# Kernel tuning notes

Measured on AMD Instinct MI355X. Metric: run time of the kernel, lower is better.

## Reference

```python
import jax, jax.numpy as jnp
import numpy as np
import math

DEPTH = 4
IN_FEATURES = 1024
LEAF_WIDTH = 256
OUT_FEATURES = 1024
BATCH = 8192
N_LEAVES = 2 ** DEPTH      # 16
N_NODES = 2 ** DEPTH - 1   # 15


def setup_inputs() -> dict:
    key = jax.random.key(0)
    ks = jax.random.split(key, 8)
    l1 = 1.0 / math.sqrt(IN_FEATURES)
    l2 = 1.0 / math.sqrt(LEAF_WIDTH)
    u = lambda k, shape, f: jax.random.uniform(k, shape, jnp.float32, -f, f)
    return {
        "x": jax.random.normal(ks[0], (BATCH, IN_FEATURES), jnp.float32),
        "node_weights": u(ks[1], (N_NODES, IN_FEATURES), l1),
        "node_biases": u(ks[2], (N_NODES, 1), l1),
        "w1s": u(ks[3], (N_LEAVES, IN_FEATURES, LEAF_WIDTH), l1),
        "b1s": u(ks[4], (N_LEAVES, LEAF_WIDTH), l1),
        "w2s": u(ks[5], (N_LEAVES, LEAF_WIDTH, OUT_FEATURES), l2),
        "b2s": u(ks[6], (N_LEAVES, OUT_FEATURES), l2),
    }


def reference(x, node_weights, node_biases, w1s, b1s, w2s, b2s):
    # Soft tree-gated routing (training_forward, soft decisions, no leak).
    B = x.shape[0]
    mixture = jnp.ones((B, N_LEAVES), dtype=x.dtype)
    for d in range(DEPTH):  # static small loop over tree depth
        plat, nxt = 2 ** d - 1, 2 ** (d + 1) - 1
        n = 2 ** d
        w = node_weights[plat:nxt]          # (n, F)
        b = node_biases[plat:nxt]           # (n, 1)
        logits = x @ w.T + b.T              # (B, n)
        be = jax.nn.sigmoid(logits)
        # interleave (1-be, be) along node axis -> (B, 2n, 1)
        mod = jnp.stack([1.0 - be, be], axis=-1).reshape(B, 2 * n, 1)
        mixture = (mixture.reshape(B, 2 * n, N_LEAVES // (2 * n)) * mod).reshape(B, N_LEAVES)
    # Per-leaf two-layer MLP, then mixture-weighted sum over leaves.
    h = jnp.einsum("bf,lfh->blh", x, w1s) + b1s[None]          # (B, L, H)
    a = jax.nn.relu(h)
    y = jnp.einsum("blh,lho->blo", a, w2s) + b2s[None]          # (B, L, O)
    return jnp.sum(y * mixture[:, :, None], axis=1)             # (B, O)
```

## Files before the change

kernel.cpp:

```cpp
#include <hip/hip_runtime.h>
#include <hip/hip_bf16.h>
#include <math.h>

#define BATCH 8192
#define INF   1024
#define LEAFW 256
#define OUTF  1024
#define NLEAF 16
#define NNODE 15
#define NTOT  4096
#define KEXT  4160

typedef __bf16 bf16;
typedef __bf16 bf16x4 __attribute__((ext_vector_type(4)));
typedef __bf16 bf16x8 __attribute__((ext_vector_type(8)));
typedef float  f32x4  __attribute__((ext_vector_type(4)));

#define BM 128
#define BN 128
#define BK 64

__global__ __launch_bounds__(256) void prep_weights_kernel(
    const float* __restrict__ w1, const float* __restrict__ w2,
    const float* __restrict__ b2s, bf16* __restrict__ W1T,
    bf16* __restrict__ W2T) {
  __shared__ float lds[64][65];
  int b = blockIdx.x;
  int t = threadIdx.x;

  if (b < 2048) {
    bool isW1 = b < 1024;
    int bb = isW1 ? b : b - 1024;
    int l = bb >> 6, rem = bb & 63;
    int rb, cb, src_ld;
    const float* src;
    if (isW1) {
      rb = (rem >> 2) * 64; cb = (rem & 3) * 64;
      src = w1 + (size_t)l * INF * LEAFW; src_ld = LEAFW;
    } else {
      rb = (rem >> 4) * 64; cb = (rem & 15) * 64;
      src = w2 + (size_t)l * LEAFW * OUTF; src_ld = OUTF;
    }
    int s4 = t & 15, r = t >> 4;
#pragma unroll
    for (int i = 0; i < 4; ++i) {
      int rr = r + 16 * i;
      float4 v = *reinterpret_cast<const float4*>(
          src + (size_t)(rb + rr) * src_ld + cb + 4 * s4);
      lds[rr][4 * s4 + 0] = v.x;
      lds[rr][4 * s4 + 1] = v.y;
      lds[rr][4 * s4 + 2] = v.z;
      lds[rr][4 * s4 + 3] = v.w;
    }
    __syncthreads();
    int s8 = t & 7, c = t >> 3;
#pragma unroll
    for (int i = 0; i < 2; ++i) {
      int cc = c + 32 * i;
      bf16x8 o;
#pragma unroll
      for (int k = 0; k < 8; ++k) o[k] = (bf16)lds[8 * s8 + k][cc];
      if (isW1)
        *reinterpret_cast<bf16x8*>(
            W1T + (size_t)(l * LEAFW + cb + cc) * INF + rb + 8 * s8) = o;
      else
        *reinterpret_cast<bf16x8*>(
            W2T + (size_t)(cb + cc) * KEXT + l * LEAFW + rb + 8 * s8) = o;
    }
  } else {
    int i = (b - 2048) * 256 + t;
    int o = i >> 6, j = i & 63;
    W2T[(size_t)o * KEXT + NTOT + j] =
        (j < NLEAF) ? (bf16)b2s[(size_t)j * OUTF + o] : (bf16)0.f;
  }
}

__global__ __launch_bounds__(256) void gating_kernel(
    const float4* __restrict__ x4, const float4* __restrict__ nw4,
    const float* __restrict__ nb, float* __restrict__ mg,
    bf16* __restrict__ Aact, bf16x4* __restrict__ Xbf4) {
  int row  = blockIdx.x * 4 + (threadIdx.x >> 6);
  int lane = threadIdx.x & 63;

  float p[NNODE];
#pragma unroll
  for (int j = 0; j < NNODE; ++j) p[j] = 0.f;
#pragma unroll
  for (int c = 0; c < INF / 256; ++c) {
    int idx = c * 64 + lane;
    float4 xv = x4[(size_t)row * (INF / 4) + idx];
#pragma unroll
    for (int j = 0; j < NNODE; ++j) {
      float4 wv = nw4[j * (INF / 4) + idx];
      p[j] += xv.x * wv.x + xv.y * wv.y + xv.z * wv.z + xv.w * wv.w;
    }
    bf16x4 o = {(bf16)xv.x, (bf16)xv.y, (bf16)xv.z, (bf16)xv.w};
    Xbf4[(size_t)row * (INF / 4) + idx] = o;
  }
#pragma unroll
  for (int j = 0; j < NNODE; ++j) {
    float v = p[j];
#pragma unroll
    for (int off = 32; off > 0; off >>= 1) v += __shfl_xor(v, off);
    p[j] = 1.f / (1.f + expf(-(v + nb[j])));
  }
  float mixv[NLEAF];
#pragma unroll
  for (int L = 0; L < NLEAF; ++L) {
    int n1 = 1 + (L >> 3), n2 = 3 + (L >> 2), n3 = 7 + (L >> 1);
    float m = ((L >> 3) & 1) ? p[0] : (1.f - p[0]);
    m *= ((L >> 2) & 1) ? p[n1] : (1.f - p[n1]);
    m *= ((L >> 1) & 1) ? p[n2] : (1.f - p[n2]);
    m *= (L & 1) ? p[n3] : (1.f - p[n3]);
    mixv[L] = m;
  }
  bf16* arow = Aact + (size_t)row * KEXT + NTOT;
  if (lane == 0) {
#pragma unroll
    for (int L = 0; L < NLEAF; ++L) {
      mg[row * NLEAF + L] = mixv[L];
      arow[L] = (bf16)mixv[L];
    }
  }
  if (lane >= 16) arow[lane] = (bf16)0.f;
}

template <int EPI>
__global__ __launch_bounds__(256, 2) void gemm_kernel(
    const bf16* __restrict__ A, int lda, const bf16* __restrict__ BT, int ldb,
    int K, const float* __restrict__ bias, const float* __restrict__ mg,
    bf16* __restrict__ outB, int ldob, float* __restrict__ outF, int ldof) {
  __shared__ __align__(16) bf16 As[BM * BK];
  __shared__ __align__(16) bf16 Bs[BN * BK];

  int t    = threadIdx.x;
  int lane = t & 63;
  int w    = t >> 6;
  int bm   = blockIdx.x * BM;
  int bn   = blockIdx.y * BN;
  int wm   = (w >> 1) * 64;
  int wn   = (w & 1) * 64;

  int sr = t >> 3;
  int sc = t & 7;
  int gc = ((sc ^ (sr & 7)) << 3);

  f32x4 acc[4][4];
#pragma unroll
  for (int i = 0; i < 4; ++i)
#pragma unroll
    for (int j = 0; j < 4; ++j) acc[i][j] = (f32x4){0.f, 0.f, 0.f, 0.f};

  for (int k0 = 0; k0 < K; k0 += BK) {
#pragma unroll
    for (int i = 0; i < 4; ++i) {
      int r = i * 32 + sr;
      __builtin_amdgcn_global_load_lds(
          (const __attribute__((address_space(1))) void*)(
              A + (size_t)(bm + r) * lda + k0 + gc),
          (__attribute__((address_space(3))) void*)((char*)As + i * 4096 +
                                                    t * 16),
          16, 0, 0);
    }
#pragma unroll
    for (int i = 0; i < 4; ++i) {
      int r = i * 32 + sr;
      __builtin_amdgcn_global_load_lds(
          (const __attribute__((address_space(1))) void*)(
              BT + (size_t)(bn + r) * ldb + k0 + gc),
          (__attribute__((address_space(3))) void*)((char*)Bs + i * 4096 +
                                                    t * 16),
          16, 0, 0);
    }
    __syncthreads();

#pragma unroll
    for (int kk = 0; kk < 2; ++kk) {
      int c = (kk * 4 + (lane >> 4)) ^ (lane & 7);
      bf16x8 af[4], bfr[4];
#pragma unroll
      for (int i = 0; i < 4; ++i) {
        int R = wm + i * 16 + (lane & 15);
        af[i] = *reinterpret_cast<const bf16x8*>(&As[R * 64 + c * 8]);
      }
#pragma unroll
      for (int j = 0; j < 4; ++j) {
        int R = wn + j * 16 + (lane & 15);
        bfr[j] = *reinterpret_cast<const bf16x8*>(&Bs[R * 64 + c * 8]);
      }
#pragma unroll
      for (int i = 0; i < 4; ++i)
#pragma unroll
        for (int j = 0; j < 4; ++j)
          acc[i][j] = __builtin_amdgcn_mfma_f32_16x16x32_bf16(
              af[i], bfr[j], acc[i][j], 0, 0, 0);
    }
    __syncthreads();
  }

  int r0 = bm + wm + ((lane >> 4) << 2);
  int c0 = bn + wn + (lane & 15);
  if (EPI == 0) {
    int leaf = (bn + wn) >> 8;
#pragma unroll
    for (int i = 0; i < 4; ++i) {
#pragma unroll
      for (int r = 0; r < 4; ++r) {
        int row = r0 + i * 16 + r;
        float g = mg[row * NLEAF + leaf];
#pragma unroll
        for (int j = 0; j < 4; ++j) {
          int col = c0 + j * 16;
          float v = acc[i][j][r] + bias[col];
          v = v > 0.f ? v : 0.f;
          outB[(size_t)row * ldob + col] = (bf16)(v * g);
        }
      }
    }
  } else {
#pragma unroll
    for (int i = 0; i < 4; ++i)
#pragma unroll
      for (int r = 0; r < 4; ++r) {
        int row = r0 + i * 16 + r;
#pragma unroll
        for (int j = 0; j < 4; ++j)
          outF[(size_t)row * ldof + (c0 + j * 16)] = acc[i][j][r];
      }
  }
}

extern "C" void kernel_launch(void* const* d_in, const int* in_sizes, int n_in,
                              void* d_out, int out_size, void* d_ws,
                              size_t ws_size, hipStream_t stream) {
  const float* x   = (const float*)d_in[0];
  const float* nw  = (const float*)d_in[1];
  const float* nb  = (const float*)d_in[2];
  const float* w1s = (const float*)d_in[3];
  const float* b1s = (const float*)d_in[4];
  const float* w2s = (const float*)d_in[5];
  const float* b2s = (const float*)d_in[6];
  float* out = (float*)d_out;

  char* ws = (char*)d_ws;
  bf16*  Xbf  = (bf16*)(ws);
  bf16*  W1T  = (bf16*)(ws + 16777216);
  bf16*  W2T  = (bf16*)(ws + 25165824);
  float* mg   = (float*)(ws + 33685504);
  bf16*  Aact = (bf16*)(ws + 34209792);

  prep_weights_kernel<<<dim3(2304), 256, 0, stream>>>(w1s, w2s, b2s, W1T, W2T);
  gating_kernel<<<dim3(BATCH / 4), 256, 0, stream>>>(
      (const float4*)x, (const float4*)nw, nb, mg, Aact, (bf16x4*)Xbf);

  gemm_kernel<0><<<dim3(BATCH / BM, NTOT / BN), 256, 0, stream>>>(
      Xbf, INF, W1T, INF, INF, b1s, mg, Aact, KEXT, nullptr, 0);
  gemm_kernel<1><<<dim3(BATCH / BM, OUTF / BN), 256, 0, stream>>>(
      Aact, KEXT, W2T, KEXT, KEXT, nullptr, nullptr, nullptr, 0, out, OUTF);
}
```

Measured before the change: 286.8 us.

## Fuse gating into weight-prep kernel and stage node weights in LDS

Merges the gating kernel into the weight-prep launch as 128 extra blocks. Each of these blocks loads all 15 node-weight vectors into LDS and then processes 64 rows, 16 per wave. This removes one kernel launch and lets the gating work overlap with the weight transposes, and node weights are read from LDS instead of being re-fetched from global memory for every row. The cost is that every block now reserves a 60KB static LDS array, which cuts occupancy for the transpose blocks. Gating parallelism also drops from 2048 blocks to 128.

```diff
diff --git a/kernel.cpp b/kernel.cpp
--- a/kernel.cpp
+++ b/kernel.cpp
@@ -20,15 +20,19 @@
 #define BN 128
 #define BK 64
 
-__global__ __launch_bounds__(256) void prep_weights_kernel(
+__global__ __launch_bounds__(256) void prep_gate_kernel(
     const float* __restrict__ w1, const float* __restrict__ w2,
     const float* __restrict__ b2s, bf16* __restrict__ W1T,
-    bf16* __restrict__ W2T) {
-  __shared__ float lds[64][65];
+    bf16* __restrict__ W2T, const float4* __restrict__ x4,
+    const float4* __restrict__ nw4, const float* __restrict__ nb,
+    float* __restrict__ mg, bf16* __restrict__ Aact,
+    bf16x4* __restrict__ Xbf4) {
+  __shared__ float lds_f[NNODE * INF];
   int b = blockIdx.x;
   int t = threadIdx.x;
 
   if (b < 2048) {
+    float(*lds)[65] = reinterpret_cast<float(*)[65]>(lds_f);
     bool isW1 = b < 1024;
     int bb = isW1 ? b : b - 1024;
     int l = bb >> 6, rem = bb & 63;
@@ -67,62 +71,72 @@
         *reinterpret_cast<bf16x8*>(
             W2T + (size_t)(cb + cc) * KEXT + l * LEAFW + rb + 8 * s8) = o;
     }
-  } else {
+  } else if (b < 2304) {
     int i = (b - 2048) * 256 + t;
     int o = i >> 6, j = i & 63;
     W2T[(size_t)o * KEXT + NTOT + j] =
         (j < NLEAF) ? (bf16)b2s[(size_t)j * OUTF + o] : (bf16)0.f;
+  } else {
+    float4* nwl = reinterpret_cast<float4*>(lds_f);
+#pragma unroll
+    for (int k = 0; k < 60; ++k) nwl[t + 256 * k] = nw4[t + 256 * k];
+    __syncthreads();
+
+    int lane = threadIdx.x & 63;
+    int rbase = (b - 2304) * 64 + (threadIdx.x >> 6) * 16;
+    for (int rr = 0; rr < 16; ++rr) {
+      int row = rbase + rr;
+      float4 xv[4];
+#pragma unroll
+      for (int c = 0; c < 4; ++c)
+        xv[c] = x4[(size_t)row * (INF / 4) + c * 64 + lane];
+#pragma unroll
+      for (int c = 0; c < 4; ++c) {
+        bf16x4 o = {(bf16)xv[c].x, (bf16)xv[c].y, (bf16)xv[c].z,
+                    (bf16)xv[c].w};
+        Xbf4[(size_t)row * (INF / 4) + c * 64 + lane] = o;
+      }
+      float p[NNODE];
+#pragma unroll
+      for (int j = 0; j < NNODE; ++j) p[j] = 0.f;
+#pragma unroll
+      for (int c = 0; c < 4; ++c) {
+        int idx = c * 64 + lane;
+#pragma unroll
+        for (int j = 0; j < NNODE; ++j) {
+          float4 wv = nwl[j * 256 + idx];
+          p[j] += xv[c].x * wv.x + xv[c].y * wv.y + xv[c].z * wv.z +
+                  xv[c].w * wv.w;
+        }
+      }
+#pragma unroll
+      for (int j = 0; j < NNODE; ++j) {
+        float v = p[j];
+#pragma unroll
+        for (int off = 32; off > 0; off >>= 1) v += __shfl_xor(v, off);
+        p[j] = 1.f / (1.f + expf(-(v + nb[j])));
+      }
+      float mixv[NLEAF];
+#pragma unroll
+      for (int L = 0; L < NLEAF; ++L) {
+        int n1 = 1 + (L >> 3), n2 = 3 + (L >> 2), n3 = 7 + (L >> 1);
+        float m = ((L >> 3) & 1) ? p[0] : (1.f - p[0]);
+        m *= ((L >> 2) & 1) ? p[n1] : (1.f - p[n1]);
+        m *= ((L >> 1) & 1) ? p[n2] : (1.f - p[n2]);
+        m *= (L & 1) ? p[n3] : (1.f - p[n3]);
+        mixv[L] = m;
+      }
+      bf16* arow = Aact + (size_t)row * KEXT + NTOT;
+      if (lane == 0) {
+#pragma unroll
+        for (int L = 0; L < NLEAF; ++L) {
+          mg[row * NLEAF + L] = mixv[L];
+          arow[L] = (bf16)mixv[L];
+        }
+      }
+      if (lane >= 16) arow[lane] = (bf16)0.f;
+    }
   }
-}
-
-__global__ __launch_bounds__(256) void gating_kernel(
-    const float4* __restrict__ x4, const float4* __restrict__ nw4,
-    const float* __restrict__ nb, float* __restrict__ mg,
-    bf16* __restrict__ Aact, bf16x4* __restrict__ Xbf4) {
-  int row  = blockIdx.x * 4 + (threadIdx.x >> 6);
-  int lane = threadIdx.x & 63;
-
-  float p[NNODE];
-#pragma unroll
-  for (int j = 0; j < NNODE; ++j) p[j] = 0.f;
-#pragma unroll
-  for (int c = 0; c < INF / 256; ++c) {
-    int idx = c * 64 + lane;
-    float4 xv = x4[(size_t)row * (INF / 4) + idx];
-#pragma unroll
-    for (int j = 0; j < NNODE; ++j) {
-      float4 wv = nw4[j * (INF / 4) + idx];
-      p[j] += xv.x * wv.x + xv.y * wv.y + xv.z * wv.z + xv.w * wv.w;
-    }
-    bf16x4 o = {(bf16)xv.x, (bf16)xv.y, (bf16)xv.z, (bf16)xv.w};
-    Xbf4[(size_t)row * (INF / 4) + idx] = o;
-  }
-#pragma unroll
-  for (int j = 0; j < NNODE; ++j) {
-    float v = p[j];
-#pragma unroll
-    for (int off = 32; off > 0; off >>= 1) v += __shfl_xor(v, off);
-    p[j] = 1.f / (1.f + expf(-(v + nb[j])));
-  }
-  float mixv[NLEAF];
-#pragma unroll
-  for (int L = 0; L < NLEAF; ++L) {
-    int n1 = 1 + (L >> 3), n2 = 3 + (L >> 2), n3 = 7 + (L >> 1);
-    float m = ((L >> 3) & 1) ? p[0] : (1.f - p[0]);
-    m *= ((L >> 2) & 1) ? p[n1] : (1.f - p[n1]);
-    m *= ((L >> 1) & 1) ? p[n2] : (1.f - p[n2]);
-    m *= (L & 1) ? p[n3] : (1.f - p[n3]);
-    mixv[L] = m;
-  }
-  bf16* arow = Aact + (size_t)row * KEXT + NTOT;
-  if (lane == 0) {
-#pragma unroll
-    for (int L = 0; L < NLEAF; ++L) {
-      mg[row * NLEAF + L] = mixv[L];
-      arow[L] = (bf16)mixv[L];
-    }
-  }
-  if (lane >= 16) arow[lane] = (bf16)0.f;
 }
 
 template <int EPI>
@@ -249,9 +263,9 @@
   float* mg   = (float*)(ws + 33685504);
   bf16*  Aact = (bf16*)(ws + 34209792);
 
-  prep_weights_kernel<<<dim3(2304), 256, 0, stream>>>(w1s, w2s, b2s, W1T, W2T);
-  gating_kernel<<<dim3(BATCH / 4), 256, 0, stream>>>(
-      (const float4*)x, (const float4*)nw, nb, mg, Aact, (bf16x4*)Xbf);
+  prep_gate_kernel<<<dim3(2432), 256, 0, stream>>>(
+      w1s, w2s, b2s, W1T, W2T, (const float4*)x, (const float4*)nw, nb, mg,
+      Aact, (bf16x4*)Xbf);
 
   gemm_kernel<0><<<dim3(BATCH / BM, NTOT / BN), 256, 0, stream>>>(
       Xbf, INF, W1T, INF, INF, b1s, mg, Aact, KEXT, nullptr, 0);
```

New measurement: 328.5 us. +14.6%, slower.
